# Kernel optimization log

Hardware: AMD Instinct MI355X
Metric: run time of the kernel (lower is better)

The kernel has to match this reference:

```python
import jax, jax.numpy as jnp
import numpy as np

SIGMA = 1e-4      # cone height (DistanceFieldPenetrationLoss sigma)
EPS = 1e-9
THRESH = 2000.0   # pen_loss[pen_loss < 2000]
WEIGHT = 0.1      # self.weight


def setup_inputs() -> dict:
    key = jax.random.key(0)
    k1, k2, k3, k4 = jax.random.split(key, 4)
    B, NV, NF, C = 16, 6890, 13776, 65536
    verts = jax.random.normal(k1, (B, NV, 3), dtype=jnp.float32)
    trans = jax.random.normal(k2, (B, 3), dtype=jnp.float32)
    faces = jax.random.randint(k3, (NF, 3), 0, NV)
    collision_idxs = jax.random.randint(k4, (B // 2, C, 2), 0, 2 * NF)
    return {"verts": verts, "trans": trans, "faces": faces,
            "collision_idxs": collision_idxs}


def _pen_distance(triangles, collision_idxs):
    # triangles: [Bp, F, 3, 3]; collision_idxs: [Bp, C, 2]
    intr_idx = collision_idxs[..., 0]
    recv_idx = collision_idxs[..., 1]
    # stand-in for the BVH's (-1)-padding / self-collision filter
    valid = (intr_idx != recv_idx).astype(triangles.dtype)            # [Bp, C]
    gather = jax.vmap(lambda t, i: t[i])
    intr = gather(triangles, intr_idx)                                # [Bp, C, 3, 3]
    recv = gather(triangles, recv_idx)                                # [Bp, C, 3, 3]
    # receiver triangle frame
    e1 = recv[..., 1, :] - recv[..., 0, :]
    e2 = recv[..., 2, :] - recv[..., 0, :]
    n = jnp.cross(e1, e2)
    n = n / (jnp.linalg.norm(n, axis=-1, keepdims=True) + EPS)        # unit normal
    c = recv.mean(axis=-2)                                            # [Bp, C, 3] centroid
    radius = jnp.linalg.norm(recv - c[..., None, :], axis=-1).max(axis=-1)  # circumscribed radius
    # conical distance field evaluated at the 3 intruder vertices
    delta = intr - c[..., None, :]                                    # [Bp, C, 3, 3]
    d = jnp.einsum('bcvk,bck->bcv', delta, n)                         # signed normal distance
    radial = jnp.linalg.norm(delta - d[..., None] * n[..., None, :], axis=-1)
    field = jax.nn.relu(-d / SIGMA) * jax.nn.relu(1.0 - radial / (radius[..., None] + EPS))
    pair_loss = (field ** 2).sum(axis=-1)                             # [Bp, C]
    return (pair_loss * valid).sum(axis=-1)                           # [Bp]


def reference(verts, trans, faces, collision_idxs):
    B, NV, _ = verts.shape
    NF = faces.shape[0]
    vertices = verts + trans[:, None, :]                              # [B, NV, 3]
    offs = (jnp.arange(B, dtype=faces.dtype) * NV)[:, None, None]
    faces_idx = (faces[None] + offs).reshape(B // 2, 2 * NF, 3)       # merge person pairs
    triangles = vertices.reshape(-1, 3)[faces_idx]                    # [B//2, 2*NF, 3, 3]
    pen = _pen_distance(triangles, collision_idxs)                    # [B//2]
    keep = (pen < THRESH).astype(pen.dtype)
    cnt = keep.sum()
    vals = (jax.nn.sigmoid(pen / THRESH) - 0.5) * keep
    loss = jnp.where(cnt > 0, vals.sum() / jnp.maximum(cnt, 1.0), 0.0) * WEIGHT
    return loss
```

## Files before the change

kernel.cpp:

```cpp
#include <hip/hip_runtime.h>
#include <math.h>

namespace {
constexpr int kB  = 16;
constexpr int kNV = 6890;
constexpr int kNF = 13776;
constexpr int kP  = kB / 2;
constexpr int kC  = 65536;
constexpr int kNB = 256;
constexpr int kPasses = 8;
}

#define SIGMA_F  1e-4f
#define EPS_F    1e-9f
#define THRESH_F 2000.0f
#define WEIGHT_F 0.1f

__device__ int      g_flag[kP]     = {};
__device__ unsigned g_count        = 0;
__device__ float    g_partials[kNB] = {};

__device__ __forceinline__ float cone_pair_loss(
    float3 r0, float3 r1, float3 r2, float3 i0, float3 i1, float3 i2) {
    float e1x = r1.x - r0.x, e1y = r1.y - r0.y, e1z = r1.z - r0.z;
    float e2x = r2.x - r0.x, e2y = r2.y - r0.y, e2z = r2.z - r0.z;
    float nx = e1y * e2z - e1z * e2y;
    float ny = e1z * e2x - e1x * e2z;
    float nz = e1x * e2y - e1y * e2x;
    float nn = sqrtf(nx * nx + ny * ny + nz * nz) + EPS_F;
    nx /= nn; ny /= nn; nz /= nn;
    float cx = (r0.x + r1.x + r2.x) / 3.0f;
    float cy = (r0.y + r1.y + r2.y) / 3.0f;
    float cz = (r0.z + r1.z + r2.z) / 3.0f;
    float r2m = 0.0f;
    {
        float dx = r0.x - cx, dy = r0.y - cy, dz = r0.z - cz;
        r2m = fmaxf(r2m, dx * dx + dy * dy + dz * dz);
        dx = r1.x - cx; dy = r1.y - cy; dz = r1.z - cz;
        r2m = fmaxf(r2m, dx * dx + dy * dy + dz * dz);
        dx = r2.x - cx; dy = r2.y - cy; dz = r2.z - cz;
        r2m = fmaxf(r2m, dx * dx + dy * dy + dz * dz);
    }
    float rad_eps = sqrtf(r2m) + EPS_F;
    float3 iv[3] = {i0, i1, i2};
    float acc = 0.0f;
#pragma unroll
    for (int k = 0; k < 3; ++k) {
        float dx = iv[k].x - cx, dy = iv[k].y - cy, dz = iv[k].z - cz;
        float d = dx * nx + dy * ny + dz * nz;
        float px = dx - d * nx, py = dy - d * ny, pz = dz - d * nz;
        float radial = sqrtf(px * px + py * py + pz * pz);
        float fa = fmaxf(-d / SIGMA_F, 0.0f);
        float fb = fmaxf(1.0f - radial / rad_eps, 0.0f);
        float fd = fa * fb;
        acc += fd * fd;
    }
    return acc;
}

__device__ __forceinline__ float eval_collision(
    int p, int2 idx,
    const float* __restrict__ verts, const int* __restrict__ faces,
    float t0x, float t0y, float t0z, float t1x, float t1y, float t1z) {
    int hi = (idx.x >= kNF) ? 1 : 0;
    int hr = (idx.y >= kNF) ? 1 : 0;
    const int* fi = faces + 3 * (idx.x - hi * kNF);
    const int* fr = faces + 3 * (idx.y - hr * kNF);
    int vi0 = fi[0], vi1 = fi[1], vi2 = fi[2];
    int vr0 = fr[0], vr1 = fr[1], vr2 = fr[2];
    size_t bi = (size_t)(2 * p + hi) * kNV;
    size_t br = (size_t)(2 * p + hr) * kNV;
    float tix = hi ? t1x : t0x, tiy = hi ? t1y : t0y, tiz = hi ? t1z : t0z;
    float trx = hr ? t1x : t0x, try_ = hr ? t1y : t0y, trz = hr ? t1z : t0z;
    const float* q;
    q = verts + (bi + vi0) * 3; float3 i0 = make_float3(q[0] + tix, q[1] + tiy, q[2] + tiz);
    q = verts + (bi + vi1) * 3; float3 i1 = make_float3(q[0] + tix, q[1] + tiy, q[2] + tiz);
    q = verts + (bi + vi2) * 3; float3 i2 = make_float3(q[0] + tix, q[1] + tiy, q[2] + tiz);
    q = verts + (br + vr0) * 3; float3 r0 = make_float3(q[0] + trx, q[1] + try_, q[2] + trz);
    q = verts + (br + vr1) * 3; float3 r1 = make_float3(q[0] + trx, q[1] + try_, q[2] + trz);
    q = verts + (br + vr2) * 3; float3 r2 = make_float3(q[0] + trx, q[1] + try_, q[2] + trz);
    float v = cone_pair_loss(r0, r1, r2, i0, i1, i2);
    return (idx.x != idx.y) ? v : 0.0f;
}

__global__ void __launch_bounds__(256)
pen_fused(const int* __restrict__ coll,
          const float* __restrict__ verts,
          const float* __restrict__ trans,
          const int* __restrict__ faces,
          float* __restrict__ out) {
    const int blk  = blockIdx.x;
    const int p    = blk & 7;
    const int base = (blk >> 3) * (kPasses * 256);
    const int2* cp = (const int2*)coll + (size_t)p * kC;

    const float t0x = trans[6 * p + 0], t0y = trans[6 * p + 1], t0z = trans[6 * p + 2];
    const float t1x = trans[6 * p + 3], t1y = trans[6 * p + 4], t1z = trans[6 * p + 5];

    __shared__ int   s_any[4];
    __shared__ int   s_stop;
    __shared__ float s_red[4];
    __shared__ float s_pen[kP];

    const int lane = threadIdx.x & 63;
    const int wid  = threadIdx.x >> 6;

    float acc = 0.0f;
    for (int s = 0; s < kPasses; ++s) {
        int2 idx = cp[base + s * 256 + threadIdx.x];
        acc += eval_collision(p, idx, verts, faces, t0x, t0y, t0z, t1x, t1y, t1z);

        int ex = __any(acc >= THRESH_F) ? 1 : 0;
        if (lane == 0) s_any[wid] = ex;
        __syncthreads();
        if (threadIdx.x == 0) {
            int any = s_any[0] | s_any[1] | s_any[2] | s_any[3];
            int f = any;
            if (any) {
                __hip_atomic_store(&g_flag[p], 1, __ATOMIC_RELAXED,
                                   __HIP_MEMORY_SCOPE_AGENT);
            } else if (s + 1 < kPasses) {
                f = __hip_atomic_load(&g_flag[p], __ATOMIC_RELAXED,
                                      __HIP_MEMORY_SCOPE_AGENT);
            }
            s_stop = f;
        }
        __syncthreads();
        if (s_stop) break;
    }

#pragma unroll
    for (int off = 32; off > 0; off >>= 1)
        acc += __shfl_down(acc, off, 64);
    if (lane == 0) s_red[wid] = acc;
    __syncthreads();
    if (threadIdx.x == 0) {
        float partial = s_red[0] + s_red[1] + s_red[2] + s_red[3];
        __hip_atomic_store(&g_partials[blk], partial, __ATOMIC_RELEASE,
                           __HIP_MEMORY_SCOPE_AGENT);
        unsigned old = __hip_atomic_fetch_add(&g_count, 1u, __ATOMIC_ACQ_REL,
                                              __HIP_MEMORY_SCOPE_AGENT);
        s_stop = (old == (unsigned)(kNB - 1));
    }
    __syncthreads();
    if (!s_stop) return;

    const int t = threadIdx.x;
    const int q = t >> 5;
    const int j = t & 31;
    float v = __hip_atomic_load(&g_partials[q + 8 * j], __ATOMIC_ACQUIRE,
                                __HIP_MEMORY_SCOPE_AGENT);
#pragma unroll
    for (int off = 16; off > 0; off >>= 1)
        v += __shfl_down(v, off, 32);
    if (j == 0) s_pen[q] = v;
    __syncthreads();
    if (t == 0) {
        float cnt = 0.0f, vals = 0.0f;
#pragma unroll
        for (int e = 0; e < kP; ++e) {
            int fl = __hip_atomic_load(&g_flag[e], __ATOMIC_RELAXED,
                                       __HIP_MEMORY_SCOPE_AGENT);
            float pq = s_pen[e];
            if (!fl && pq < THRESH_F) {
                cnt += 1.0f;
                vals += 1.0f / (1.0f + expf(-pq / THRESH_F)) - 0.5f;
            }
        }
        float loss = (cnt > 0.0f) ? (vals / fmaxf(cnt, 1.0f)) : 0.0f;
        out[0] = loss * WEIGHT_F;
#pragma unroll
        for (int e = 0; e < kP; ++e)
            __hip_atomic_store(&g_flag[e], 0, __ATOMIC_RELAXED,
                               __HIP_MEMORY_SCOPE_AGENT);
        __hip_atomic_store(&g_count, 0u, __ATOMIC_RELEASE,
                           __HIP_MEMORY_SCOPE_AGENT);
    }
}

extern "C" void kernel_launch(void* const* d_in, const int* in_sizes, int n_in,
                              void* d_out, int out_size, void* d_ws, size_t ws_size,
                              hipStream_t stream) {
    const float* verts = (const float*)d_in[0];
    const float* trans = (const float*)d_in[1];
    const int*   faces = (const int*)d_in[2];
    const int*   coll  = (const int*)d_in[3];
    (void)d_ws; (void)ws_size; (void)in_sizes; (void)n_in; (void)out_size;
    pen_fused<<<kNB, 256, 0, stream>>>(coll, verts, trans, faces, (float*)d_out);
}
```

Measured before the change: 74.11 us.

## Make early-exit and reduction per-wave with per-pair atomic accumulation

Removes block-level barriers from the early-exit loop so each wavefront independently checks the threshold and the global flag. Replaces per-block partials and the single final gather with per-pair float atomicAdd, plus per-pair wave counters and a done counter that elects the finalizing wave. This cuts barrier stalls and the final reduction step, but adds global atomics per wave and a summation order that is no longer deterministic.

```diff
diff --git a/kernel.cpp b/kernel.cpp
--- a/kernel.cpp
+++ b/kernel.cpp
@@ -8,7 +8,11 @@
 constexpr int kP  = kB / 2;
 constexpr int kC  = 65536;
 constexpr int kNB = 256;
-constexpr int kPasses = 8;
+constexpr int kTPB = 256;
+constexpr int kWPB = kTPB / 64;
+constexpr int kWavesPerPair = (kNB / kP) * kWPB;
+constexpr int kLanesPerPair = kWavesPerPair * 64;
+constexpr int kPasses = kC / kLanesPerPair;
 }
 
 #define SIGMA_F  1e-4f
@@ -16,9 +20,10 @@
 #define THRESH_F 2000.0f
 #define WEIGHT_F 0.1f
 
-__device__ int      g_flag[kP]     = {};
-__device__ unsigned g_count        = 0;
-__device__ float    g_partials[kNB] = {};
+__device__ int      g_flag[kP] = {};
+__device__ float    g_pen[kP]  = {};
+__device__ unsigned g_cnt[kP]  = {};
+__device__ unsigned g_done     = 0;
 
 __device__ __forceinline__ float cone_pair_loss(
     float3 r0, float3 r1, float3 r2, float3 i0, float3 i1, float3 i2) {
@@ -91,77 +96,54 @@
           float* __restrict__ out) {
     const int blk  = blockIdx.x;
     const int p    = blk & 7;
-    const int base = (blk >> 3) * (kPasses * 256);
+    const int lane = threadIdx.x & 63;
+    const int wq   = (blk >> 3) * kWPB + (threadIdx.x >> 6);
     const int2* cp = (const int2*)coll + (size_t)p * kC;
 
     const float t0x = trans[6 * p + 0], t0y = trans[6 * p + 1], t0z = trans[6 * p + 2];
     const float t1x = trans[6 * p + 3], t1y = trans[6 * p + 4], t1z = trans[6 * p + 5];
 
-    __shared__ int   s_any[4];
-    __shared__ int   s_stop;
-    __shared__ float s_red[4];
-    __shared__ float s_pen[kP];
-
-    const int lane = threadIdx.x & 63;
-    const int wid  = threadIdx.x >> 6;
-
     float acc = 0.0f;
     for (int s = 0; s < kPasses; ++s) {
-        int2 idx = cp[base + s * 256 + threadIdx.x];
+        int2 idx = cp[s * kLanesPerPair + wq * 64 + lane];
         acc += eval_collision(p, idx, verts, faces, t0x, t0y, t0z, t1x, t1y, t1z);
-
-        int ex = __any(acc >= THRESH_F) ? 1 : 0;
-        if (lane == 0) s_any[wid] = ex;
-        __syncthreads();
-        if (threadIdx.x == 0) {
-            int any = s_any[0] | s_any[1] | s_any[2] | s_any[3];
-            int f = any;
-            if (any) {
+        if (__any(acc >= THRESH_F)) {
+            if (lane == 0)
                 __hip_atomic_store(&g_flag[p], 1, __ATOMIC_RELAXED,
                                    __HIP_MEMORY_SCOPE_AGENT);
-            } else if (s + 1 < kPasses) {
-                f = __hip_atomic_load(&g_flag[p], __ATOMIC_RELAXED,
-                                      __HIP_MEMORY_SCOPE_AGENT);
-            }
-            s_stop = f;
+            break;
         }
-        __syncthreads();
-        if (s_stop) break;
+        if (s + 1 < kPasses &&
+            __hip_atomic_load(&g_flag[p], __ATOMIC_RELAXED,
+                              __HIP_MEMORY_SCOPE_AGENT))
+            break;
     }
 
 #pragma unroll
     for (int off = 32; off > 0; off >>= 1)
         acc += __shfl_down(acc, off, 64);
-    if (lane == 0) s_red[wid] = acc;
-    __syncthreads();
-    if (threadIdx.x == 0) {
-        float partial = s_red[0] + s_red[1] + s_red[2] + s_red[3];
-        __hip_atomic_store(&g_partials[blk], partial, __ATOMIC_RELEASE,
-                           __HIP_MEMORY_SCOPE_AGENT);
-        unsigned old = __hip_atomic_fetch_add(&g_count, 1u, __ATOMIC_ACQ_REL,
-                                              __HIP_MEMORY_SCOPE_AGENT);
-        s_stop = (old == (unsigned)(kNB - 1));
+
+    int fin = 0;
+    if (lane == 0) {
+        atomicAdd(&g_pen[p], acc);
+        unsigned o = __hip_atomic_fetch_add(&g_cnt[p], 1u, __ATOMIC_ACQ_REL,
+                                            __HIP_MEMORY_SCOPE_AGENT);
+        if (o == (unsigned)(kWavesPerPair - 1)) {
+            unsigned d = __hip_atomic_fetch_add(&g_done, 1u, __ATOMIC_ACQ_REL,
+                                                __HIP_MEMORY_SCOPE_AGENT);
+            fin = (d == (unsigned)(kP - 1));
+        }
     }
-    __syncthreads();
-    if (!s_stop) return;
+    if (__shfl(fin, 0, 64) == 0) return;
 
-    const int t = threadIdx.x;
-    const int q = t >> 5;
-    const int j = t & 31;
-    float v = __hip_atomic_load(&g_partials[q + 8 * j], __ATOMIC_ACQUIRE,
-                                __HIP_MEMORY_SCOPE_AGENT);
-#pragma unroll
-    for (int off = 16; off > 0; off >>= 1)
-        v += __shfl_down(v, off, 32);
-    if (j == 0) s_pen[q] = v;
-    __syncthreads();
-    if (t == 0) {
+    if (lane == 0) {
         float cnt = 0.0f, vals = 0.0f;
 #pragma unroll
         for (int e = 0; e < kP; ++e) {
             int fl = __hip_atomic_load(&g_flag[e], __ATOMIC_RELAXED,
                                        __HIP_MEMORY_SCOPE_AGENT);
-            float pq = s_pen[e];
+            float pq = __hip_atomic_load(&g_pen[e], __ATOMIC_RELAXED,
+                                         __HIP_MEMORY_SCOPE_AGENT);
             if (!fl && pq < THRESH_F) {
                 cnt += 1.0f;
                 vals += 1.0f / (1.0f + expf(-pq / THRESH_F)) - 0.5f;
@@ -170,10 +152,15 @@
         float loss = (cnt > 0.0f) ? (vals / fmaxf(cnt, 1.0f)) : 0.0f;
         out[0] = loss * WEIGHT_F;
 #pragma unroll
-        for (int e = 0; e < kP; ++e)
+        for (int e = 0; e < kP; ++e) {
             __hip_atomic_store(&g_flag[e], 0, __ATOMIC_RELAXED,
                                __HIP_MEMORY_SCOPE_AGENT);
-        __hip_atomic_store(&g_count, 0u, __ATOMIC_RELEASE,
+            __hip_atomic_store(&g_pen[e], 0.0f, __ATOMIC_RELAXED,
+                               __HIP_MEMORY_SCOPE_AGENT);
+            __hip_atomic_store(&g_cnt[e], 0u, __ATOMIC_RELAXED,
+                               __HIP_MEMORY_SCOPE_AGENT);
+        }
+        __hip_atomic_store(&g_done, 0u, __ATOMIC_RELEASE,
                            __HIP_MEMORY_SCOPE_AGENT);
     }
 }
@@ -186,5 +173,5 @@
     const int*   faces = (const int*)d_in[2];
     const int*   coll  = (const int*)d_in[3];
     (void)d_ws; (void)ws_size; (void)in_sizes; (void)n_in; (void)out_size;
-    pen_fused<<<kNB, 256, 0, stream>>>(coll, verts, trans, faces, (float*)d_out);
+    pen_fused<<<kNB, kTPB, 0, stream>>>(coll, verts, trans, faces, (float*)d_out);
 }
```

Result: slower. 115.8 us (+56.3%).
